# Performance work log

Hardware: AMD Instinct MI355X
Metric: run time of the kernel (lower is better)

Reference implementation:

```python
import jax, jax.numpy as jnp
import numpy as np
import math

D_MODEL = 1024
NUM_HEADS = 16
D_K = D_MODEL // NUM_HEADS


def setup_inputs() -> dict:
    key = jax.random.key(0)
    ks = jax.random.split(key, 7)
    B, S = 2, 2048
    scale = 1.0 / math.sqrt(D_MODEL)
    inp = {
        "q": jax.random.normal(ks[0], (B, S, D_MODEL), dtype=jnp.float32),
        "k": jax.random.normal(ks[1], (B, S, D_MODEL), dtype=jnp.float32),
        "v": jax.random.normal(ks[2], (B, S, D_MODEL), dtype=jnp.float32),
        # Source module reuses q_linear for q, k, and v projections, so only
        # Wq/bq are needed for the input projections; out projection separate.
        "Wq": jax.random.normal(ks[3], (D_MODEL, D_MODEL), dtype=jnp.float32) * scale,
        "bq": jnp.zeros((D_MODEL,), dtype=jnp.float32),
        "Wo": jax.random.normal(ks[4], (D_MODEL, D_MODEL), dtype=jnp.float32) * scale,
        "bo": jnp.zeros((D_MODEL,), dtype=jnp.float32),
    }
    return inp


def _attention(q, k, v, Wq, bq, Wo, bo):
    B, S, _ = q.shape

    def proj(x):
        # [B,S,D] -> [B,H,S,d_k]
        y = jnp.einsum("bsd,de->bse", x, Wq) + bq
        return y.reshape(B, S, NUM_HEADS, D_K).transpose(0, 2, 1, 3)

    qh, kh, vh = proj(q), proj(k), proj(v)
    # scores: [B,H,S,S]
    scores = jnp.einsum("bhsd,bhtd->bhst", qh, kh) / math.sqrt(D_K)
    attn = jax.nn.softmax(scores, axis=-1)
    # dropout: eval-mode identity
    out = jnp.einsum("bhst,bhtd->bhsd", attn, vh)  # [B,H,S,d_k]
    out = out.transpose(0, 2, 1, 3).reshape(B, S, D_MODEL)
    return jnp.einsum("bsd,de->bse", out, Wo) + bo


def reference(q, k, v, Wq, bq, Wo, bo):
    return _attention(q, k, v, Wq, bq, Wo, bo)
```

## Files before the change

kernel.cpp:

```cpp
#include <hip/hip_runtime.h>
#include <hip/hip_bf16.h>

typedef unsigned short u16;
typedef unsigned int   u32;
typedef __attribute__((ext_vector_type(8))) short bf16x8;
typedef __attribute__((ext_vector_type(4))) float f32x4;
typedef __attribute__((ext_vector_type(16))) float f32x16;

#define SEQ     2048
#define DM      1024
#define NH      16
#define DKH     64
#define PER_SRC 4194304

__device__ __forceinline__ u16 f2bf(float f) {
    union { float f; u32 u; } c; c.f = f;
    return (u16)((c.u + 0x7fffu + ((c.u >> 16) & 1u)) >> 16);
}

__device__ __forceinline__ u32 cvt_pk_bf16(float lo, float hi) {
    u32 r;
    asm("v_cvt_pk_bf16_f32 %0, %1, %2" : "=v"(r) : "v"(lo), "v"(hi));
    return r;
}

__device__ __forceinline__ void gload_lds16(const void* g, void* l) {
    __builtin_amdgcn_global_load_lds((__attribute__((address_space(1))) void*)g,
                                     (__attribute__((address_space(3))) void*)l,
                                     16, 0, 0);
}

__global__ void cast_qkv(const float* __restrict__ q, const float* __restrict__ k,
                         const float* __restrict__ v, u16* __restrict__ xb) {
    const float* src = (blockIdx.y == 0) ? q : (blockIdx.y == 1) ? k : v;
    u16* dst = xb + (size_t)blockIdx.y * PER_SRC;
    size_t i = ((size_t)blockIdx.x * 256 + threadIdx.x) * 8;
    float4 a = *(const float4*)(src + i);
    float4 b = *(const float4*)(src + i + 4);
    bf16x8 o;
    o[0] = (short)f2bf(a.x); o[1] = (short)f2bf(a.y);
    o[2] = (short)f2bf(a.z); o[3] = (short)f2bf(a.w);
    o[4] = (short)f2bf(b.x); o[5] = (short)f2bf(b.y);
    o[6] = (short)f2bf(b.z); o[7] = (short)f2bf(b.w);
    *(bf16x8*)(dst + i) = o;
}

__global__ void wtrans(const float* __restrict__ Wq, const float* __restrict__ Wo,
                       u16* __restrict__ Wqt, u16* __restrict__ Wot) {
    const float* W = blockIdx.y ? Wo : Wq;
    u16* Wt       = blockIdx.y ? Wot : Wqt;
    int k0 = (blockIdx.x & 15) * 64;
    int n0 = (blockIdx.x >> 4) * 64;
    __shared__ __align__(16) float t[64][68];
    int tid = threadIdx.x;
    int r = tid >> 2, cs = (tid & 3) * 16;
    #pragma unroll
    for (int j = 0; j < 4; ++j) {
        float4 vv = *(const float4*)(W + (size_t)(k0 + r) * DM + n0 + cs + j * 4);
        *(float4*)&t[r][cs + j * 4] = vv;
    }
    __syncthreads();
    bf16x8 o0, o1;
    #pragma unroll
    for (int j = 0; j < 8; ++j) o0[j] = (short)f2bf(t[cs + j][r]);
    #pragma unroll
    for (int j = 0; j < 8; ++j) o1[j] = (short)f2bf(t[cs + 8 + j][r]);
    u16* dst = Wt + (size_t)(n0 + r) * DM + k0 + cs;
    *(bf16x8*)(dst)     = o0;
    *(bf16x8*)(dst + 8) = o1;
}

__global__ void vtrans(const u16* __restrict__ vh, u16* __restrict__ vt) {
    int bh = blockIdx.y, st = blockIdx.x;
    __shared__ u16 t[64][72];
    int tid = threadIdx.x;
    int r = tid >> 2, cs = (tid & 3) * 16;
    const u16* src = vh + ((size_t)bh * SEQ + st * 64 + r) * DKH + cs;
    bf16x8 v0 = *(const bf16x8*)(src);
    bf16x8 v1 = *(const bf16x8*)(src + 8);
    #pragma unroll
    for (int j = 0; j < 8; ++j) { t[r][cs + j] = (u16)v0[j]; t[r][cs + 8 + j] = (u16)v1[j]; }
    __syncthreads();
    bf16x8 o0, o1;
    #pragma unroll
    for (int j = 0; j < 8; ++j) o0[j] = (short)t[cs + j][r];
    #pragma unroll
    for (int j = 0; j < 8; ++j) o1[j] = (short)t[cs + 8 + j][r];
    u16* dst = vt + ((size_t)bh * DKH + r) * SEQ + st * 64 + cs;
    *(bf16x8*)(dst)     = o0;
    *(bf16x8*)(dst + 8) = o1;
}

template<int MODE>
__global__ __launch_bounds__(256)
void gemm_bt(const u16* __restrict__ Abase, const u16* __restrict__ Bt,
             const float* __restrict__ bias, void* __restrict__ outbase)
{
    __shared__ __align__(16) u16 Alds[128 * 64];
    __shared__ __align__(16) u16 Blds[128 * 64];

    const int tid  = threadIdx.x;
    const int wave = tid >> 6;
    const int lane = tid & 63;
    const int low4 = lane & 15;
    const int quad = lane >> 4;
    const int m0 = (blockIdx.x >> 3) * 128;
    const int n0 = (blockIdx.x & 7) * 128;
    const int wm = (wave >> 1) * 64, wn = (wave & 1) * 64;

    const u16* A = Abase + (size_t)blockIdx.z * PER_SRC;

    f32x4 acc[4][4] = {};

    for (int kt = 0; kt < DM / 64; ++kt) {
        #pragma unroll
        for (int it = 0; it < 4; ++it) {
            int seg  = it * 256 + tid;
            int row  = seg >> 3;
            int slot = seg & 7;
            int ss   = slot ^ (row & 7);
            const u16* srcA;
            if (MODE == 0) {
                srcA = A + (size_t)(m0 + row) * DM + kt * 64 + ss * 8;
            } else {
                int m = m0 + row;
                srcA = A + (((size_t)((m >> 11) * NH + kt)) * SEQ + (m & (SEQ - 1))) * DKH + ss * 8;
            }
            gload_lds16(srcA, &Alds[(it * 256 + wave * 64) * 8]);
            gload_lds16(Bt + (size_t)(n0 + row) * DM + kt * 64 + ss * 8,
                        &Blds[(it * 256 + wave * 64) * 8]);
        }
        __syncthreads();
        #pragma unroll
        for (int kk = 0; kk < 2; ++kk) {
            bf16x8 af[4], bfr[4];
            #pragma unroll
            for (int mi = 0; mi < 4; ++mi) {
                int row = wm + mi * 16 + low4;
                af[mi] = *(const bf16x8*)&Alds[row * 64 + (((kk * 4 + quad) ^ (row & 7)) * 8)];
            }
            #pragma unroll
            for (int ni = 0; ni < 4; ++ni) {
                int row = wn + ni * 16 + low4;
                bfr[ni] = *(const bf16x8*)&Blds[row * 64 + (((kk * 4 + quad) ^ (row & 7)) * 8)];
            }
            #pragma unroll
            for (int mi = 0; mi < 4; ++mi)
                #pragma unroll
                for (int ni = 0; ni < 4; ++ni)
                    acc[mi][ni] = __builtin_amdgcn_mfma_f32_16x16x32_bf16(
                        af[mi], bfr[ni], acc[mi][ni], 0, 0, 0);
        }
        __syncthreads();
    }

    #pragma unroll
    for (int mi = 0; mi < 4; ++mi) {
        #pragma unroll
        for (int ni = 0; ni < 4; ++ni) {
            int n = n0 + wn + ni * 16 + low4;
            float bv = bias[n];
            #pragma unroll
            for (int j = 0; j < 4; ++j) {
                int m = m0 + wm + mi * 16 + quad * 4 + j;
                float val = acc[mi][ni][j] + bv;
                if (MODE == 0) {
                    u16* dst = (u16*)outbase + (size_t)blockIdx.z * PER_SRC;
                    int b = m >> 11, s = m & (SEQ - 1);
                    int h = n >> 6, dd = n & 63;
                    dst[(size_t)(b * NH + h) * (SEQ * DKH) + (size_t)s * DKH + dd] = f2bf(val);
                } else {
                    ((float*)outbase)[(size_t)m * DM + n] = val;
                }
            }
        }
    }
}

__global__ __launch_bounds__(256, 2)
void attn(const u16* __restrict__ qh, const u16* __restrict__ kh,
          const u16* __restrict__ vt, u16* __restrict__ aoh)
{
    __shared__ __align__(16) u16 lds[2][8192];

    const int tid  = threadIdx.x;
    const int w    = tid >> 6;
    const int lane = tid & 63;
    const int l31  = lane & 31;
    const int hi   = lane >> 5;

    int bid = blockIdx.x;
    int lid = (bid & 7) * 64 + (bid >> 3);
    const int qt = lid & 15;
    const int bh = lid >> 4;

    const int qbase = qt * 128 + w * 32;
    const int q_row = qbase + l31;

    const float SC = 0.18033688f;

    bf16x8 qf[4];
    #pragma unroll
    for (int c = 0; c < 4; ++c)
        qf[c] = *(const bf16x8*)&qh[((size_t)bh * SEQ + q_row) * DKH + c * 16 + hi * 8];

    float m_r = -1e30f, l_r = 0.f;
    f32x16 ot[2] = {};

#define STAGE(buf, kt_)                                                                 \
    {                                                                                   \
        _Pragma("unroll")                                                               \
        for (int it = 0; it < 2; ++it) {                                                \
            int seg  = it * 256 + tid;                                                  \
            int row  = seg >> 3;                                                        \
            int slot = seg & 7;                                                         \
            int ss   = slot ^ (row & 7);                                                \
            gload_lds16(kh + ((size_t)bh * SEQ + (kt_) * 64 + row) * DKH + ss * 8,      \
                        &lds[buf][(it * 256 + w * 64) * 8]);                            \
            gload_lds16(vt + ((size_t)bh * DKH + row) * SEQ + (kt_) * 64 + ss * 8,      \
                        &lds[buf][4096 + (it * 256 + w * 64) * 8]);                     \
        }                                                                               \
    }

    STAGE(0, 0);
    __syncthreads();

    int cur = 0;
    for (int kt = 0; kt < SEQ / 64; ++kt) {
        if (kt + 1 < SEQ / 64) STAGE(cur ^ 1, kt + 1);

        const u16* Klds = &lds[cur][0];
        const u16* Vlds = &lds[cur][4096];

        f32x16 st[2];
        #pragma unroll
        for (int T = 0; T < 2; ++T) {
            f32x16 acc = {};
            __builtin_amdgcn_s_setprio(1);
            #pragma unroll
            for (int c = 0; c < 4; ++c) {
                int row = T * 32 + l31;
                bf16x8 kf = *(const bf16x8*)&Klds[row * 64 + (((c * 2 + hi) ^ (row & 7)) * 8)];
                acc = __builtin_amdgcn_mfma_f32_32x32x16_bf16(kf, qf[c], acc, 0, 0, 0);
            }
            __builtin_amdgcn_s_setprio(0);
            st[T] = acc;
        }

        float mx[8];
        #pragma unroll
        for (int r = 0; r < 8; ++r)
            mx[r] = fmaxf(fmaxf(st[0][r], st[0][r + 8]),
                          fmaxf(st[1][r], st[1][r + 8]));
        float t0 = fmaxf(fmaxf(mx[0], mx[1]), mx[2]);
        float t1 = fmaxf(fmaxf(mx[3], mx[4]), mx[5]);
        float t2 = fmaxf(mx[6], mx[7]);
        float lmax = fmaxf(fmaxf(t0, t1), t2);
        float mloc = fmaxf(lmax, __shfl_xor(lmax, 32)) * SC;

        float mnew = fmaxf(m_r, mloc);
        if (!__all(mloc <= m_r + 11.5f)) {
            float fac = __builtin_amdgcn_exp2f(m_r - mnew);
            m_r = mnew;
            l_r *= fac;
            #pragma unroll
            for (int dt = 0; dt < 2; ++dt)
                #pragma unroll
                for (int r = 0; r < 16; ++r) ot[dt][r] *= fac;
        }

        float nm = -m_r;
        float rs0 = 0.f, rs1 = 0.f, rs2 = 0.f, rs3 = 0.f;
        #pragma unroll
        for (int T = 0; T < 2; ++T)
            #pragma unroll
            for (int r = 0; r < 16; r += 4) {
                float p0 = __builtin_amdgcn_exp2f(fmaf(st[T][r],     SC, nm));
                float p1 = __builtin_amdgcn_exp2f(fmaf(st[T][r + 1], SC, nm));
                float p2 = __builtin_amdgcn_exp2f(fmaf(st[T][r + 2], SC, nm));
                float p3 = __builtin_amdgcn_exp2f(fmaf(st[T][r + 3], SC, nm));
                st[T][r] = p0; st[T][r + 1] = p1; st[T][r + 2] = p2; st[T][r + 3] = p3;
                rs0 += p0; rs1 += p1; rs2 += p2; rs3 += p3;
            }
        float rsum = (rs0 + rs1) + (rs2 + rs3);
        l_r += rsum + __shfl_xor(rsum, 32);

        u32 pk[2][8];
        #pragma unroll
        for (int T = 0; T < 2; ++T)
            #pragma unroll
            for (int g = 0; g < 8; ++g)
                pk[T][g] = cvt_pk_bf16(st[T][2 * g], st[T][2 * g + 1]);

        __builtin_amdgcn_s_setprio(1);
        #pragma unroll
        for (int dt = 0; dt < 2; ++dt)
            #pragma unroll
            for (int c = 0; c < 4; ++c) {
                int row = dt * 32 + l31;
                const char* vrow = (const char*)&Vlds[row * 64];
                union { bf16x8 v; uint2 d[2]; } vf;
                vf.d[0] = *(const uint2*)(vrow + (((c * 2)     ^ (row & 7)) * 16) + hi * 8);
                vf.d[1] = *(const uint2*)(vrow + (((c * 2 + 1) ^ (row & 7)) * 16) + hi * 8);
                union { bf16x8 v; u32 u[4]; } pf;
                int T = c >> 1, g0 = (c & 1) * 4;
                pf.u[0] = pk[T][g0];     pf.u[1] = pk[T][g0 + 1];
                pf.u[2] = pk[T][g0 + 2]; pf.u[3] = pk[T][g0 + 3];
                ot[dt] = __builtin_amdgcn_mfma_f32_32x32x16_bf16(vf.v, pf.v, ot[dt], 0, 0, 0);
            }
        __builtin_amdgcn_s_setprio(0);

        __syncthreads();
        cur ^= 1;
    }

    float inv = 1.0f / l_r;
    u16* tile = &lds[0][0] + w * 2048;
    #pragma unroll
    for (int dt = 0; dt < 2; ++dt)
        #pragma unroll
        for (int g = 0; g < 4; ++g) {
            u32 w0 = cvt_pk_bf16(ot[dt][4 * g] * inv,     ot[dt][4 * g + 1] * inv);
            u32 w1 = cvt_pk_bf16(ot[dt][4 * g + 2] * inv, ot[dt][4 * g + 3] * inv);
            int d0 = 8 * g + 4 * hi + 32 * dt;
            int byteoff = l31 * 128 + ((d0 * 2) ^ ((l31 & 7) << 4));
            uint2 pr; pr.x = w0; pr.y = w1;
            *(uint2*)((char*)tile + byteoff) = pr;
        }
    const size_t gbase = ((size_t)bh * SEQ + qbase) * DKH;
    #pragma unroll
    for (int p = 0; p < 4; ++p) {
        int q = p * 8 + (lane >> 3);
        int byteoff = q * 128 + (((lane & 7) * 16) ^ ((q & 7) << 4));
        bf16x8 val = *(const bf16x8*)((const char*)tile + byteoff);
        *(bf16x8*)&aoh[gbase + p * 512 + lane * 8] = val;
    }
#undef STAGE
}

extern "C" void kernel_launch(void* const* d_in, const int* in_sizes, int n_in,
                              void* d_out, int out_size, void* d_ws, size_t ws_size,
                              hipStream_t stream)
{
    const float* q  = (const float*)d_in[0];
    const float* k  = (const float*)d_in[1];
    const float* v  = (const float*)d_in[2];
    const float* Wq = (const float*)d_in[3];
    const float* bq = (const float*)d_in[4];
    const float* Wo = (const float*)d_in[5];
    const float* bo = (const float*)d_in[6];

    char* ws = (char*)d_ws;
    u16* xb  = (u16*)(ws);
    u16* wqt = (u16*)(ws + 25165824);
    u16* wot = (u16*)(ws + 27262976);
    u16* qh  = (u16*)(ws + 29360128);
    u16* kh  = qh + PER_SRC;
    u16* vh  = kh + PER_SRC;
    u16* vt  = (u16*)(ws);
    u16* aoh = (u16*)(ws + 8388608);

    cast_qkv<<<dim3(2048, 3), dim3(256), 0, stream>>>(q, k, v, xb);
    wtrans<<<dim3(256, 2), dim3(256), 0, stream>>>(Wq, Wo, wqt, wot);
    gemm_bt<0><<<dim3(256, 1, 3), dim3(256), 0, stream>>>(xb, wqt, bq, (void*)qh);
    vtrans<<<dim3(32, 32), dim3(256), 0, stream>>>(vh, vt);
    attn<<<dim3(512), dim3(256), 0, stream>>>(qh, kh, vt, aoh);
    gemm_bt<1><<<dim3(256), dim3(256), 0, stream>>>(aoh, wot, bo, d_out);
}
```

Baseline: 144.6 us.

## Split attention over two key halves with a merge kernel

The attention kernel is templated on a split flag. With enough workspace it launches 1024 blocks, each covering half of the key sequence, and writes fp32 partial outputs plus running max and sum to workspace. A new merge kernel then combines them into bf16 head outputs. Separately, the V transpose now writes elements in a permuted order so the PV MFMA can load each V fragment with one 16-byte LDS read instead of two 8-byte reads. The split aims to raise occupancy and parallelism across the GPU's compute units, at the cost of extra fp32 partial traffic and one more kernel launch.

```diff
diff --git a/kernel.cpp b/kernel.cpp
--- a/kernel.cpp
+++ b/kernel.cpp
@@ -12,6 +12,19 @@
 #define NH      16
 #define DKH     64
 #define PER_SRC 4194304
+
+#define OFF_VT   0u
+#define OFF_AOH  8388608u
+#define OFF_WQT  25165824u
+#define OFF_WOT  27262976u
+#define OFF_QH   29360128u
+#define OFF_KH   37748736u
+#define OFF_VH   46137344u
+#define OFF_PO   54525952u
+#define OFF_PML  88080384u
+#define NEED_WS  89128960u
+#define PART_O_F 4194304
+#define PART_ML_F 131072
 
 __device__ __forceinline__ u16 f2bf(float f) {
     union { float f; u32 u; } c; c.f = f;
@@ -86,9 +99,15 @@
     for (int j = 0; j < 8; ++j) o0[j] = (short)t[cs + j][r];
     #pragma unroll
     for (int j = 0; j < 8; ++j) o1[j] = (short)t[cs + 8 + j][r];
+    bf16x8 w0, w1;
+    #pragma unroll
+    for (int j = 0; j < 4; ++j) {
+        w0[j] = o0[j];     w0[4 + j] = o1[j];
+        w1[j] = o0[4 + j]; w1[4 + j] = o1[4 + j];
+    }
     u16* dst = vt + ((size_t)bh * DKH + r) * SEQ + st * 64 + cs;
-    *(bf16x8*)(dst)     = o0;
-    *(bf16x8*)(dst + 8) = o1;
+    *(bf16x8*)(dst)     = w0;
+    *(bf16x8*)(dst + 8) = w1;
 }
 
 template<int MODE>
@@ -177,9 +196,11 @@
     }
 }
 
+template<int SPLIT>
 __global__ __launch_bounds__(256, 2)
 void attn(const u16* __restrict__ qh, const u16* __restrict__ kh,
-          const u16* __restrict__ vt, u16* __restrict__ aoh)
+          const u16* __restrict__ vt, u16* __restrict__ aoh,
+          float* __restrict__ pO, float* __restrict__ pml)
 {
     __shared__ __align__(16) u16 lds[2][8192];
 
@@ -193,6 +214,9 @@
     int lid = (bid & 7) * 64 + (bid >> 3);
     const int qt = lid & 15;
     const int bh = lid >> 4;
+    const int part = SPLIT ? blockIdx.y : 0;
+    const int kt0  = part * 16;
+    const int nkt  = SPLIT ? 16 : 32;
 
     const int qbase = qt * 128 + w * 32;
     const int q_row = qbase + l31;
@@ -222,12 +246,12 @@
         }                                                                               \
     }
 
-    STAGE(0, 0);
+    STAGE(0, kt0);
     __syncthreads();
 
     int cur = 0;
-    for (int kt = 0; kt < SEQ / 64; ++kt) {
-        if (kt + 1 < SEQ / 64) STAGE(cur ^ 1, kt + 1);
+    for (int ki = 0; ki < nkt; ++ki) {
+        if (ki + 1 < nkt) STAGE(cur ^ 1, kt0 + ki + 1);
 
         const u16* Klds = &lds[cur][0];
         const u16* Vlds = &lds[cur][4096];
@@ -298,15 +322,12 @@
             #pragma unroll
             for (int c = 0; c < 4; ++c) {
                 int row = dt * 32 + l31;
-                const char* vrow = (const char*)&Vlds[row * 64];
-                union { bf16x8 v; uint2 d[2]; } vf;
-                vf.d[0] = *(const uint2*)(vrow + (((c * 2)     ^ (row & 7)) * 16) + hi * 8);
-                vf.d[1] = *(const uint2*)(vrow + (((c * 2 + 1) ^ (row & 7)) * 16) + hi * 8);
+                bf16x8 vf = *(const bf16x8*)&Vlds[row * 64 + (((c * 2 + hi) ^ (row & 7)) * 8)];
                 union { bf16x8 v; u32 u[4]; } pf;
                 int T = c >> 1, g0 = (c & 1) * 4;
                 pf.u[0] = pk[T][g0];     pf.u[1] = pk[T][g0 + 1];
                 pf.u[2] = pk[T][g0 + 2]; pf.u[3] = pk[T][g0 + 3];
-                ot[dt] = __builtin_amdgcn_mfma_f32_32x32x16_bf16(vf.v, pf.v, ot[dt], 0, 0, 0);
+                ot[dt] = __builtin_amdgcn_mfma_f32_32x32x16_bf16(vf, pf.v, ot[dt], 0, 0, 0);
             }
         __builtin_amdgcn_s_setprio(0);
 
@@ -314,28 +335,89 @@
         cur ^= 1;
     }
 
-    float inv = 1.0f / l_r;
-    u16* tile = &lds[0][0] + w * 2048;
-    #pragma unroll
-    for (int dt = 0; dt < 2; ++dt)
-        #pragma unroll
-        for (int g = 0; g < 4; ++g) {
-            u32 w0 = cvt_pk_bf16(ot[dt][4 * g] * inv,     ot[dt][4 * g + 1] * inv);
-            u32 w1 = cvt_pk_bf16(ot[dt][4 * g + 2] * inv, ot[dt][4 * g + 3] * inv);
-            int d0 = 8 * g + 4 * hi + 32 * dt;
-            int byteoff = l31 * 128 + ((d0 * 2) ^ ((l31 & 7) << 4));
-            uint2 pr; pr.x = w0; pr.y = w1;
-            *(uint2*)((char*)tile + byteoff) = pr;
-        }
-    const size_t gbase = ((size_t)bh * SEQ + qbase) * DKH;
-    #pragma unroll
-    for (int p = 0; p < 4; ++p) {
-        int q = p * 8 + (lane >> 3);
-        int byteoff = q * 128 + (((lane & 7) * 16) ^ ((q & 7) << 4));
-        bf16x8 val = *(const bf16x8*)((const char*)tile + byteoff);
-        *(bf16x8*)&aoh[gbase + p * 512 + lane * 8] = val;
+    if (SPLIT == 0) {
+        float inv = 1.0f / l_r;
+        u16* tile = &lds[0][0] + w * 2048;
+        #pragma unroll
+        for (int dt = 0; dt < 2; ++dt)
+            #pragma unroll
+            for (int g = 0; g < 4; ++g) {
+                u32 w0 = cvt_pk_bf16(ot[dt][4 * g] * inv,     ot[dt][4 * g + 1] * inv);
+                u32 w1 = cvt_pk_bf16(ot[dt][4 * g + 2] * inv, ot[dt][4 * g + 3] * inv);
+                int d0 = 8 * g + 4 * hi + 32 * dt;
+                int byteoff = l31 * 128 + ((d0 * 2) ^ ((l31 & 7) << 4));
+                uint2 pr; pr.x = w0; pr.y = w1;
+                *(uint2*)((char*)tile + byteoff) = pr;
+            }
+        const size_t gbase = ((size_t)bh * SEQ + qbase) * DKH;
+        #pragma unroll
+        for (int p = 0; p < 4; ++p) {
+            int q = p * 8 + (lane >> 3);
+            int byteoff = q * 128 + (((lane & 7) * 16) ^ ((q & 7) << 4));
+            bf16x8 val = *(const bf16x8*)((const char*)tile + byteoff);
+            *(bf16x8*)&aoh[gbase + p * 512 + lane * 8] = val;
+        }
+    } else {
+        float* ftile = (float*)&lds[0][0] + w * 2048;
+        #pragma unroll
+        for (int dt = 0; dt < 2; ++dt)
+            #pragma unroll
+            for (int g = 0; g < 4; ++g) {
+                int d0 = 8 * g + 4 * hi + 32 * dt;
+                int slot = (d0 >> 2) ^ (l31 & 15);
+                f32x4 vv;
+                vv[0] = ot[dt][4 * g];     vv[1] = ot[dt][4 * g + 1];
+                vv[2] = ot[dt][4 * g + 2]; vv[3] = ot[dt][4 * g + 3];
+                *(f32x4*)((char*)ftile + l31 * 256 + slot * 16) = vv;
+            }
+        float* po = pO + (size_t)part * PART_O_F + ((size_t)bh * SEQ + qbase) * DKH;
+        #pragma unroll
+        for (int p = 0; p < 8; ++p) {
+            int q = p * 4 + (lane >> 4);
+            int chunk = lane & 15;
+            f32x4 val = *(const f32x4*)((const char*)ftile + q * 256 + ((chunk ^ (q & 15)) * 16));
+            *(f32x4*)&po[(size_t)q * DKH + chunk * 4] = val;
+        }
+        if (hi == 0) {
+            float2 ml; ml.x = m_r; ml.y = l_r;
+            *(float2*)&pml[(size_t)part * PART_ML_F + ((size_t)bh * SEQ + qbase + l31) * 2] = ml;
+        }
     }
 #undef STAGE
+}
+
+__global__ __launch_bounds__(256)
+void attn_merge(const float* __restrict__ pO, const float* __restrict__ pml,
+                u16* __restrict__ aoh)
+{
+    int tid = threadIdx.x;
+    int bh = blockIdx.x >> 5;
+    int qb = blockIdx.x & 31;
+    int ql = tid >> 2;
+    int dc = tid & 3;
+    size_t row = (size_t)bh * SEQ + qb * 64 + ql;
+
+    float2 ml1 = *(const float2*)&pml[row * 2];
+    float2 ml2 = *(const float2*)&pml[PART_ML_F + row * 2];
+    float m  = fmaxf(ml1.x, ml2.x);
+    float w1 = __builtin_amdgcn_exp2f(ml1.x - m);
+    float w2 = __builtin_amdgcn_exp2f(ml2.x - m);
+    float inv = 1.0f / (ml1.y * w1 + ml2.y * w2);
+    float a1 = w1 * inv, a2 = w2 * inv;
+
+    const f32x4* r1 = (const f32x4*)&pO[row * DKH + dc * 16];
+    const f32x4* r2 = (const f32x4*)&pO[PART_O_F + row * DKH + dc * 16];
+    u16* dst = aoh + row * DKH + dc * 16;
+    u16 outv[16];
+    #pragma unroll
+    for (int i = 0; i < 4; ++i) {
+        f32x4 x = r1[i], y = r2[i];
+        #pragma unroll
+        for (int j = 0; j < 4; ++j)
+            outv[i * 4 + j] = f2bf(x[j] * a1 + y[j] * a2);
+    }
+    *(bf16x8*)(dst)     = *(bf16x8*)&outv[0];
+    *(bf16x8*)(dst + 8) = *(bf16x8*)&outv[8];
 }
 
 extern "C" void kernel_launch(void* const* d_in, const int* in_sizes, int n_in,
@@ -352,18 +434,25 @@
 
     char* ws = (char*)d_ws;
     u16* xb  = (u16*)(ws);
-    u16* wqt = (u16*)(ws + 25165824);
-    u16* wot = (u16*)(ws + 27262976);
-    u16* qh  = (u16*)(ws + 29360128);
-    u16* kh  = qh + PER_SRC;
-    u16* vh  = kh + PER_SRC;
-    u16* vt  = (u16*)(ws);
-    u16* aoh = (u16*)(ws + 8388608);
+    u16* wqt = (u16*)(ws + OFF_WQT);
+    u16* wot = (u16*)(ws + OFF_WOT);
+    u16* qh  = (u16*)(ws + OFF_QH);
+    u16* kh  = (u16*)(ws + OFF_KH);
+    u16* vh  = (u16*)(ws + OFF_VH);
+    u16* vt  = (u16*)(ws + OFF_VT);
+    u16* aoh = (u16*)(ws + OFF_AOH);
+    float* pO  = (float*)(ws + OFF_PO);
+    float* pml = (float*)(ws + OFF_PML);
 
     cast_qkv<<<dim3(2048, 3), dim3(256), 0, stream>>>(q, k, v, xb);
     wtrans<<<dim3(256, 2), dim3(256), 0, stream>>>(Wq, Wo, wqt, wot);
     gemm_bt<0><<<dim3(256, 1, 3), dim3(256), 0, stream>>>(xb, wqt, bq, (void*)qh);
     vtrans<<<dim3(32, 32), dim3(256), 0, stream>>>(vh, vt);
-    attn<<<dim3(512), dim3(256), 0, stream>>>(qh, kh, vt, aoh);
+    if (ws_size >= (size_t)NEED_WS) {
+        attn<1><<<dim3(512, 2), dim3(256), 0, stream>>>(qh, kh, vt, aoh, pO, pml);
+        attn_merge<<<dim3(1024), dim3(256), 0, stream>>>(pO, pml, aoh);
+    } else {
+        attn<0><<<dim3(512), dim3(256), 0, stream>>>(qh, kh, vt, aoh, pO, pml);
+    }
     gemm_bt<1><<<dim3(256), dim3(256), 0, stream>>>(aoh, wot, bo, d_out);
 }
```

Result: no change. 146.1 us (+1.0%).
